# Kernel optimization log

Hardware: AMD Instinct MI355X
Metric: run time of the kernel (lower is better)

Reference implementation:

```python
import jax, jax.numpy as jnp
import numpy as np
import math

B, S, D, H = 1, 4096, 1024, 16
HD = D // H  # head_dim = 64


def setup_inputs() -> dict:
    key = jax.random.key(0)
    ks = jax.random.split(key, 6)
    x = jax.random.normal(ks[0], (B, S, D), dtype=jnp.float32)
    # Llama-style rotary frequencies: theta = 10000^{-2i/head_dim}
    inv_freq = 1.0 / (10000.0 ** (jnp.arange(0, HD, 2, dtype=jnp.float32) / HD))  # (HD/2,)
    t = jnp.arange(S, dtype=jnp.float32)
    freqs = jnp.outer(t, inv_freq)  # (S, HD/2)
    cos = jnp.cos(freqs)
    sin = jnp.sin(freqs)
    # additive causal mask (S, S): 0 on/below diagonal, -inf above
    mask = jnp.where(jnp.tril(jnp.ones((S, S), dtype=bool)), 0.0, -jnp.inf).astype(jnp.float32)
    scale = 1.0 / math.sqrt(D)
    wq = jax.random.normal(ks[1], (D, D), dtype=jnp.float32) * scale
    wk = jax.random.normal(ks[2], (D, D), dtype=jnp.float32) * scale
    wv = jax.random.normal(ks[3], (D, D), dtype=jnp.float32) * scale
    wo = jax.random.normal(ks[4], (D, D), dtype=jnp.float32) * scale
    return {"x": x, "cos": cos, "sin": sin, "mask": mask,
            "wq": wq, "wk": wk, "wv": wv, "wo": wo, "start_pos": 0}


def _rope(t, cos, sin):
    # t: (b, s, h, hd); cos/sin: (s, hd/2). Interleaved-pair complex rotation.
    b, s, h, hd = t.shape
    tr = t.reshape(b, s, h, hd // 2, 2)
    te, to = tr[..., 0], tr[..., 1]
    c = cos[None, :, None, :]
    sn = sin[None, :, None, :]
    oe = te * c - to * sn
    oo = te * sn + to * c
    return jnp.stack([oe, oo], axis=-1).reshape(b, s, h, hd)


def reference(x, cos, sin, mask, wq, wk, wv, wo, start_pos):
    b, s, d = x.shape
    h, hd = H, HD
    # Linear layers: y = x @ W.T (torch nn.Linear convention, W is (out,in))
    xq = (x @ wq.T).reshape(b, s, h, hd)
    xk = (x @ wk.T).reshape(b, s, h, hd)
    xv = (x @ wv.T).reshape(b, s, h, hd)
    xq = _rope(xq, cos, sin)
    xk = _rope(xk, cos, sin)
    # (b, h, s, hd)
    xq = xq.transpose(0, 2, 1, 3)
    xk = xk.transpose(0, 2, 1, 3)
    xv = xv.transpose(0, 2, 1, 3)
    scores = jnp.einsum('bhqd,bhkd->bhqk', xq, xk) / math.sqrt(hd)
    scores = scores + mask[None, None, :, :]
    attn = jax.nn.softmax(scores.astype(jnp.float32), axis=-1).astype(xq.dtype)
    out = jnp.einsum('bhqk,bhkd->bhqd', attn, xv)
    out = out.transpose(0, 2, 1, 3).reshape(b, s, d)
    return out @ wo.T
```

## Files before the change

kernel.cpp:

```cpp
#include <hip/hip_runtime.h>
#include <hip/hip_bf16.h>
#include <math.h>

typedef __bf16 bf16;
typedef __bf16 bf16x4 __attribute__((ext_vector_type(4)));
typedef __bf16 bf16x8 __attribute__((ext_vector_type(8)));
typedef float floatx4 __attribute__((ext_vector_type(4)));
typedef short short4v __attribute__((ext_vector_type(4)));

#define S_LEN 4096
#define DM 1024
#define NH 16
#define HD 64

#define GM 4096
#define GN 1024
#define GK 1024
#define FST 68

#define GLDS16(gp, lp) __builtin_amdgcn_global_load_lds( \
    (const __attribute__((address_space(1))) void*)(gp), \
    (__attribute__((address_space(3))) void*)(lp), 16, 0, 0)

__global__ void cvt_bf16(const float* __restrict__ x,  const float* __restrict__ wq,
                         const float* __restrict__ wk, const float* __restrict__ wv,
                         const float* __restrict__ wo, bf16* __restrict__ dst)
{
    size_t i4 = ((size_t)blockIdx.x * 256 + threadIdx.x) * 4;
    const float* src; size_t off;
    const size_t M1 = (size_t)1 << 20;
    if      (i4 < 4 * M1) { src = x;  off = i4;          }
    else if (i4 < 5 * M1) { src = wq; off = i4 - 4 * M1; }
    else if (i4 < 6 * M1) { src = wk; off = i4 - 5 * M1; }
    else if (i4 < 7 * M1) { src = wv; off = i4 - 6 * M1; }
    else                  { src = wo; off = i4 - 7 * M1; }
    float4 v = *(const float4*)(src + off);
    bf16x4 o = { (bf16)v.x, (bf16)v.y, (bf16)v.z, (bf16)v.w };
    *(bf16x4*)(&dst[i4]) = o;
}

template <typename CT>
__launch_bounds__(256)
__global__ void gemm_bt3(const bf16* __restrict__ A,
                         const bf16* __restrict__ B0, const bf16* __restrict__ B1,
                         const bf16* __restrict__ B2,
                         CT* __restrict__ C0, CT* __restrict__ C1, CT* __restrict__ C2)
{
    const int bz = blockIdx.z;
    const bf16* __restrict__ B = (bz == 0) ? B0 : (bz == 1 ? B1 : B2);
    CT* __restrict__ C         = (bz == 0) ? C0 : (bz == 1 ? C1 : C2);

    const int tid  = threadIdx.x;
    const int wave = tid >> 6;
    const int lane = tid & 63;
    const int wm   = (wave >> 1) * 64;
    const int wn   = (wave & 1) * 64;
    const int lrow = lane >> 4;
    const int lcol = lane & 15;

    const int m0 = blockIdx.y * 128;
    const int n0 = blockIdx.x * 128;

    __shared__ __align__(16) bf16 As[128 * 64];
    __shared__ __align__(16) bf16 Bs[128 * 64];

    floatx4 acc[4][4];
    #pragma unroll
    for (int i = 0; i < 4; i++)
        #pragma unroll
        for (int j = 0; j < 4; j++) acc[i][j] = (floatx4){0.f, 0.f, 0.f, 0.f};

    const bf16* ga0 = A + (size_t)(m0 + wave * 32 + (lane >> 3)) * GK + (lane & 7) * 8;
    const bf16* gb0 = B + (size_t)(n0 + wave * 32 + (lane >> 3)) * GK + (lane & 7) * 8;
    bf16* la = &As[(wave * 32) * 64];
    bf16* lb = &Bs[(wave * 32) * 64];

    for (int kt = 0; kt < GK; kt += 64) {
        #pragma unroll
        for (int i = 0; i < 4; i++) {
            GLDS16(ga0 + kt + (size_t)i * 8 * GK, la + i * 8 * 64);
            GLDS16(gb0 + kt + (size_t)i * 8 * GK, lb + i * 8 * 64);
        }
        __syncthreads();
        #pragma unroll
        for (int ks = 0; ks < 2; ks++) {
            bf16x8 af[4], bfr[4];
            #pragma unroll
            for (int t = 0; t < 4; t++) {
                af[t]  = *(const bf16x8*)(&As[(wm + t * 16 + lcol) * 64 + ks * 32 + lrow * 8]);
                bfr[t] = *(const bf16x8*)(&Bs[(wn + t * 16 + lcol) * 64 + ks * 32 + lrow * 8]);
            }
            #pragma unroll
            for (int mt = 0; mt < 4; mt++)
                #pragma unroll
                for (int nt = 0; nt < 4; nt++)
                    acc[mt][nt] = __builtin_amdgcn_mfma_f32_16x16x32_bf16(af[mt], bfr[nt], acc[mt][nt], 0, 0, 0);
        }
        __syncthreads();
    }

    #pragma unroll
    for (int mt = 0; mt < 4; mt++)
        #pragma unroll
        for (int nt = 0; nt < 4; nt++)
            #pragma unroll
            for (int r = 0; r < 4; r++) {
                int row = m0 + wm + mt * 16 + lrow * 4 + r;
                int col = n0 + wn + nt * 16 + lcol;
                C[(size_t)row * GN + col] = (CT)(acc[mt][nt][r]);
            }
}

__global__ void rope_kernel(bf16* __restrict__ Q, bf16* __restrict__ Kp,
                            const float* __restrict__ cosp, const float* __restrict__ sinp)
{
    int idx = blockIdx.x * 256 + threadIdx.x;
    int s = idx >> 9;
    int r = idx & 511;
    int h = r >> 5;
    int i = r & 31;
    float c  = cosp[s * 32 + i];
    float sn = sinp[s * 32 + i];
    int base = s * DM + h * 64 + 2 * i;
    float qe = (float)Q[base], qo = (float)Q[base + 1];
    Q[base]      = (bf16)(qe * c - qo * sn);
    Q[base + 1]  = (bf16)(qe * sn + qo * c);
    float ke = (float)Kp[base], ko = (float)Kp[base + 1];
    Kp[base]     = (bf16)(ke * c - ko * sn);
    Kp[base + 1] = (bf16)(ke * sn + ko * c);
}

__global__ void vtrans_kernel(const bf16* __restrict__ V, bf16* __restrict__ VT)
{
    __shared__ bf16 T[64 * 70];
    const int tid = threadIdx.x;
    const int s0  = blockIdx.x * 64;
    const int h   = blockIdx.y;
    #pragma unroll
    for (int i = 0; i < 2; i++) {
        int idx = i * 256 + tid;
        int r   = idx >> 3;
        int c   = (idx & 7) * 8;
        *(uint4*)(&T[r * 70 + c]) = *(const uint4*)(&V[(size_t)(s0 + r) * DM + h * 64 + c]);
    }
    __syncthreads();
    #pragma unroll
    for (int i = 0; i < 2; i++) {
        int idx = i * 256 + tid;
        int d   = idx >> 3;
        int c0  = (idx & 7) * 8;
        bf16x8 o;
        #pragma unroll
        for (int j = 0; j < 8; j++) o[j] = T[(c0 + j) * 70 + d];
        *(bf16x8*)(&VT[(size_t)(h * 64 + d) * S_LEN + s0 + c0]) = o;
    }
}

__launch_bounds__(256, 4)
__global__ void flash_attn(const bf16* __restrict__ Q, const bf16* __restrict__ K,
                           const bf16* __restrict__ VT,
                           float* __restrict__ O0, float* __restrict__ O1,
                           float* __restrict__ L0, float* __restrict__ L1)
{
    const int pi   = blockIdx.x >> 1;
    const int p    = blockIdx.x & 1;
    const int h    = blockIdx.y;
    const int tid  = threadIdx.x;
    const int wave = tid >> 6;
    const int lane = tid & 63;
    const int lrow = lane >> 4;
    const int lcol = lane & 15;

    const int qtA = pi;
    const int qtB = 63 - pi;

    float* __restrict__ Op = p ? O1 : O0;
    float* __restrict__ Lp = p ? L1 : L0;

    __shared__ __align__(16) bf16 Ks[2][64 * FST];
    __shared__ __align__(16) bf16 Vs[2][64 * FST];

    const float sc2 = 0.125f * 1.44269504088896340736f;

    const int q0A = qtA * 64 + wave * 16;
    const int q0B = qtB * 64 + wave * 16;

    const bf16* qpA = Q + (size_t)(q0A + lcol) * DM + h * HD;
    const bf16* qpB = Q + (size_t)(q0B + lcol) * DM + h * HD;
    bf16x8 qfA[2], qfB[2];
    qfA[0] = *(const bf16x8*)(qpA + 0 + lrow * 8);
    qfA[1] = *(const bf16x8*)(qpA + 32 + lrow * 8);
    qfB[0] = *(const bf16x8*)(qpB + 0 + lrow * 8);
    qfB[1] = *(const bf16x8*)(qpB + 32 + lrow * 8);

    float lA = 0.f, lB = 0.f;
    floatx4 oaccA[4], oaccB[4];
    #pragma unroll
    for (int nt = 0; nt < 4; nt++) {
        oaccA[nt] = (floatx4){0.f, 0.f, 0.f, 0.f};
        oaccB[nt] = (floatx4){0.f, 0.f, 0.f, 0.f};
    }

    const int  srow = tid >> 3;
    const int  sch  = (tid & 7) * 8;
    const bf16* kp  = K  + (size_t)srow * DM + h * HD + sch;
    const bf16* vp  = VT + (size_t)(h * HD + srow) * S_LEN + sch;
    const int  wof  = srow * FST + sch;

    {
        size_t ko = (size_t)p * 64 * DM;
        size_t vo = (size_t)p * 64;
        uint4 a = *(const uint4*)(kp + ko);
        uint4 b = *(const uint4*)(kp + ko + (size_t)32 * DM);
        uint4 c = *(const uint4*)(vp + vo);
        uint4 d = *(const uint4*)(vp + vo + (size_t)32 * S_LEN);
        *(uint4*)(&Ks[0][wof])            = a;
        *(uint4*)(&Ks[0][wof + 32 * FST]) = b;
        *(uint4*)(&Vs[0][wof])            = c;
        *(uint4*)(&Vs[0][wof + 32 * FST]) = d;
    }
    __syncthreads();

    uint4 kr0, kr1, vr0, vr1;
    for (int t = p; t <= qtB; t += 2) {
        const int  cur  = ((t - p) >> 1) & 1;
        const bool more = (t + 2 <= qtB);
        const bool actA = (t <= qtA);

        if (more) {
            size_t ko = (size_t)(t + 2) * 64 * DM;
            size_t vo = (size_t)(t + 2) * 64;
            kr0 = *(const uint4*)(kp + ko);
            kr1 = *(const uint4*)(kp + ko + (size_t)32 * DM);
            vr0 = *(const uint4*)(vp + vo);
            vr1 = *(const uint4*)(vp + vo + (size_t)32 * S_LEN);
        }

        short4v pbA[4], pbB[4];
        const bool diagA = (t == qtA);
        const bool diagB = (t == qtB);
        #pragma unroll
        for (int nt = 0; nt < 4; nt++) {
            floatx4 zB = (floatx4){0.f, 0.f, 0.f, 0.f};
            floatx4 zA = (floatx4){0.f, 0.f, 0.f, 0.f};
            #pragma unroll
            for (int ks = 0; ks < 2; ks++) {
                bf16x8 kf = *(const bf16x8*)(&Ks[cur][(nt * 16 + lcol) * FST + ks * 32 + lrow * 8]);
                zB = __builtin_amdgcn_mfma_f32_16x16x32_bf16(kf, qfB[ks], zB, 0, 0, 0);
                if (actA)
                    zA = __builtin_amdgcn_mfma_f32_16x16x32_bf16(kf, qfA[ks], zA, 0, 0, 0);
            }
            if (diagB) {
                #pragma unroll
                for (int r = 0; r < 4; r++) {
                    int kg = t * 64 + nt * 16 + lrow * 4 + r;
                    float pr = exp2f(zB[r] * sc2);
                    if (kg > q0B + lcol) pr = 0.f;
                    zB[r] = pr; lB += pr;
                }
            } else {
                #pragma unroll
                for (int r = 0; r < 4; r++) {
                    float pr = exp2f(zB[r] * sc2);
                    zB[r] = pr; lB += pr;
                }
            }
            bf16x4 pvB = { (bf16)zB[0], (bf16)zB[1], (bf16)zB[2], (bf16)zB[3] };
            pbB[nt] = __builtin_bit_cast(short4v, pvB);
            if (actA) {
                if (diagA) {
                    #pragma unroll
                    for (int r = 0; r < 4; r++) {
                        int kg = t * 64 + nt * 16 + lrow * 4 + r;
                        float pr = exp2f(zA[r] * sc2);
                        if (kg > q0A + lcol) pr = 0.f;
                        zA[r] = pr; lA += pr;
                    }
                } else {
                    #pragma unroll
                    for (int r = 0; r < 4; r++) {
                        float pr = exp2f(zA[r] * sc2);
                        zA[r] = pr; lA += pr;
                    }
                }
                bf16x4 pvA = { (bf16)zA[0], (bf16)zA[1], (bf16)zA[2], (bf16)zA[3] };
                pbA[nt] = __builtin_bit_cast(short4v, pvA);
            }
        }

        #pragma unroll
        for (int nt = 0; nt < 4; nt++)
            #pragma unroll
            for (int kt = 0; kt < 4; kt++) {
                bf16x4 va = *(const bf16x4*)(&Vs[cur][(nt * 16 + lcol) * FST + kt * 16 + lrow * 4]);
                short4v vas = __builtin_bit_cast(short4v, va);
                oaccB[nt] = __builtin_amdgcn_mfma_f32_16x16x16bf16_1k(vas, pbB[kt], oaccB[nt], 0, 0, 0);
                if (actA)
                    oaccA[nt] = __builtin_amdgcn_mfma_f32_16x16x16bf16_1k(vas, pbA[kt], oaccA[nt], 0, 0, 0);
            }

        if (more) {
            int nxt = cur ^ 1;
            *(uint4*)(&Ks[nxt][wof])            = kr0;
            *(uint4*)(&Ks[nxt][wof + 32 * FST]) = kr1;
            *(uint4*)(&Vs[nxt][wof])            = vr0;
            *(uint4*)(&Vs[nxt][wof + 32 * FST]) = vr1;
        }
        __syncthreads();
    }

    lA += __shfl_xor(lA, 16, 64);
    lA += __shfl_xor(lA, 32, 64);
    lB += __shfl_xor(lB, 16, 64);
    lB += __shfl_xor(lB, 32, 64);
    if (lrow == 0) {
        Lp[h * S_LEN + q0A + lcol] = lA;
        Lp[h * S_LEN + q0B + lcol] = lB;
    }
    #pragma unroll
    for (int nt = 0; nt < 4; nt++) {
        *(floatx4*)(&Op[(size_t)(q0A + lcol) * DM + h * HD + nt * 16 + lrow * 4]) = oaccA[nt];
        *(floatx4*)(&Op[(size_t)(q0B + lcol) * DM + h * HD + nt * 16 + lrow * 4]) = oaccB[nt];
    }
}

__global__ void combine_kernel(const float* __restrict__ O0, const float* __restrict__ O1,
                               const float* __restrict__ L0, const float* __restrict__ L1,
                               bf16* __restrict__ Aw)
{
    int i4 = (blockIdx.x * 256 + threadIdx.x) * 4;
    int q = i4 >> 10;
    int c = i4 & 1023;
    int h = c >> 6;
    float rl = 1.f / (L0[h * S_LEN + q] + L1[h * S_LEN + q]);
    float4 a = *(const float4*)(O0 + i4);
    float4 b = *(const float4*)(O1 + i4);
    bf16x4 o = { (bf16)((a.x + b.x) * rl), (bf16)((a.y + b.y) * rl),
                 (bf16)((a.z + b.z) * rl), (bf16)((a.w + b.w) * rl) };
    *(bf16x4*)(&Aw[i4]) = o;
}

extern "C" void kernel_launch(void* const* d_in, const int* in_sizes, int n_in,
                              void* d_out, int out_size, void* d_ws, size_t ws_size,
                              hipStream_t stream) {
    const float* x    = (const float*)d_in[0];
    const float* cosp = (const float*)d_in[1];
    const float* sinp = (const float*)d_in[2];
    const float* wq   = (const float*)d_in[4];
    const float* wk   = (const float*)d_in[5];
    const float* wv   = (const float*)d_in[6];
    const float* wo   = (const float*)d_in[7];
    float* out = (float*)d_out;

    const size_t SD = (size_t)S_LEN * DM;
    const size_t DD = (size_t)DM * DM;
    bf16* xb  = (bf16*)d_ws;
    bf16* wqb = xb + SD;
    bf16* wkb = wqb + DD;
    bf16* wvb = wkb + DD;
    bf16* wob = wvb + DD;
    bf16* Qw  = wob + DD;
    bf16* Kw  = Qw + SD;
    bf16* Vw  = Kw + SD;
    bf16* Aw  = Vw + SD;
    bf16* VTw = Aw + SD;
    float* O0f = (float*)(VTw + SD);
    float* O1f = O0f + SD;
    float* L0f = O1f + SD;
    float* L1f = L0f + (size_t)S_LEN * NH;

    cvt_bf16<<<8192, 256, 0, stream>>>(x, wq, wk, wv, wo, xb);
    gemm_bt3<bf16><<<dim3(GN / 128, GM / 128, 3), 256, 0, stream>>>(
        xb, wqb, wkb, wvb, Qw, Kw, Vw);
    rope_kernel<<<(S_LEN * NH * 32) / 256, 256, 0, stream>>>(Qw, Kw, cosp, sinp);
    vtrans_kernel<<<dim3(S_LEN / 64, NH), 256, 0, stream>>>(Vw, VTw);
    flash_attn<<<dim3(64, NH), 256, 0, stream>>>(Qw, Kw, VTw, O0f, O1f, L0f, L1f);
    combine_kernel<<<S_LEN * DM / 1024, 256, 0, stream>>>(O0f, O1f, L0f, L1f, Aw);
    gemm_bt3<float><<<dim3(GN / 128, GM / 128, 1), 256, 0, stream>>>(
        Aw, wob, wob, wob, out, out, out);
}
```

Baseline: 306.9 us.

## Fuse bf16 conversion, RoPE, V transpose and split combine into GEMM kernels

Removes the separate fp32-to-bf16 conversion, RoPE, V-transpose and split-combine kernels. The QKV GEMM now loads fp32 inputs and converts them while staging to padded LDS, applies RoPE in its epilogue using lane shuffles, and writes V already transposed. The output GEMM merges the two flash partials and normalises by L during its A-tile load. This saves launches and intermediate memory traffic, but gives up the async global_load_lds path and reads twice the bytes (fp32) per tile, and each weight tile is reconverted by many blocks.

```diff
diff --git a/kernel.cpp b/kernel.cpp
--- a/kernel.cpp
+++ b/kernel.cpp
@@ -16,39 +16,24 @@
 #define GM 4096
 #define GN 1024
 #define GK 1024
+#define LDST 72
 #define FST 68
 
-#define GLDS16(gp, lp) __builtin_amdgcn_global_load_lds( \
-    (const __attribute__((address_space(1))) void*)(gp), \
-    (__attribute__((address_space(3))) void*)(lp), 16, 0, 0)
-
-__global__ void cvt_bf16(const float* __restrict__ x,  const float* __restrict__ wq,
-                         const float* __restrict__ wk, const float* __restrict__ wv,
-                         const float* __restrict__ wo, bf16* __restrict__ dst)
-{
-    size_t i4 = ((size_t)blockIdx.x * 256 + threadIdx.x) * 4;
-    const float* src; size_t off;
-    const size_t M1 = (size_t)1 << 20;
-    if      (i4 < 4 * M1) { src = x;  off = i4;          }
-    else if (i4 < 5 * M1) { src = wq; off = i4 - 4 * M1; }
-    else if (i4 < 6 * M1) { src = wk; off = i4 - 5 * M1; }
-    else if (i4 < 7 * M1) { src = wv; off = i4 - 6 * M1; }
-    else                  { src = wo; off = i4 - 7 * M1; }
-    float4 v = *(const float4*)(src + off);
-    bf16x4 o = { (bf16)v.x, (bf16)v.y, (bf16)v.z, (bf16)v.w };
-    *(bf16x4*)(&dst[i4]) = o;
-}
-
-template <typename CT>
+__device__ __forceinline__ bf16x8 cvt8(float4 a, float4 b) {
+    return (bf16x8){ (bf16)a.x, (bf16)a.y, (bf16)a.z, (bf16)a.w,
+                     (bf16)b.x, (bf16)b.y, (bf16)b.z, (bf16)b.w };
+}
+
 __launch_bounds__(256)
-__global__ void gemm_bt3(const bf16* __restrict__ A,
-                         const bf16* __restrict__ B0, const bf16* __restrict__ B1,
-                         const bf16* __restrict__ B2,
-                         CT* __restrict__ C0, CT* __restrict__ C1, CT* __restrict__ C2)
+__global__ void gemm_qkv(const float* __restrict__ x,
+                         const float* __restrict__ wq, const float* __restrict__ wk,
+                         const float* __restrict__ wv,
+                         const float* __restrict__ cosp, const float* __restrict__ sinp,
+                         bf16* __restrict__ Qw, bf16* __restrict__ Kw,
+                         bf16* __restrict__ VTw)
 {
     const int bz = blockIdx.z;
-    const bf16* __restrict__ B = (bz == 0) ? B0 : (bz == 1 ? B1 : B2);
-    CT* __restrict__ C         = (bz == 0) ? C0 : (bz == 1 ? C1 : C2);
+    const float* __restrict__ B = (bz == 0) ? wq : (bz == 1 ? wk : wv);
 
     const int tid  = threadIdx.x;
     const int wave = tid >> 6;
@@ -61,8 +46,8 @@
     const int m0 = blockIdx.y * 128;
     const int n0 = blockIdx.x * 128;
 
-    __shared__ __align__(16) bf16 As[128 * 64];
-    __shared__ __align__(16) bf16 Bs[128 * 64];
+    __shared__ __align__(16) bf16 As[128 * LDST];
+    __shared__ __align__(16) bf16 Bs[128 * LDST];
 
     floatx4 acc[4][4];
     #pragma unroll
@@ -70,16 +55,18 @@
         #pragma unroll
         for (int j = 0; j < 4; j++) acc[i][j] = (floatx4){0.f, 0.f, 0.f, 0.f};
 
-    const bf16* ga0 = A + (size_t)(m0 + wave * 32 + (lane >> 3)) * GK + (lane & 7) * 8;
-    const bf16* gb0 = B + (size_t)(n0 + wave * 32 + (lane >> 3)) * GK + (lane & 7) * 8;
-    bf16* la = &As[(wave * 32) * 64];
-    bf16* lb = &Bs[(wave * 32) * 64];
-
     for (int kt = 0; kt < GK; kt += 64) {
         #pragma unroll
         for (int i = 0; i < 4; i++) {
-            GLDS16(ga0 + kt + (size_t)i * 8 * GK, la + i * 8 * 64);
-            GLDS16(gb0 + kt + (size_t)i * 8 * GK, lb + i * 8 * 64);
+            int idx = i * 256 + tid;
+            int row = idx >> 3;
+            int ch  = (idx & 7) * 8;
+            const float* ap = &x[(size_t)(m0 + row) * GK + kt + ch];
+            const float* bp = &B[(size_t)(n0 + row) * GK + kt + ch];
+            float4 a0 = *(const float4*)(ap), a1 = *(const float4*)(ap + 4);
+            float4 b0 = *(const float4*)(bp), b1 = *(const float4*)(bp + 4);
+            *(bf16x8*)(&As[row * LDST + ch]) = cvt8(a0, a1);
+            *(bf16x8*)(&Bs[row * LDST + ch]) = cvt8(b0, b1);
         }
         __syncthreads();
         #pragma unroll
@@ -87,8 +74,8 @@
             bf16x8 af[4], bfr[4];
             #pragma unroll
             for (int t = 0; t < 4; t++) {
-                af[t]  = *(const bf16x8*)(&As[(wm + t * 16 + lcol) * 64 + ks * 32 + lrow * 8]);
-                bfr[t] = *(const bf16x8*)(&Bs[(wn + t * 16 + lcol) * 64 + ks * 32 + lrow * 8]);
+                af[t]  = *(const bf16x8*)(&As[(wm + t * 16 + lcol) * LDST + ks * 32 + lrow * 8]);
+                bfr[t] = *(const bf16x8*)(&Bs[(wn + t * 16 + lcol) * LDST + ks * 32 + lrow * 8]);
             }
             #pragma unroll
             for (int mt = 0; mt < 4; mt++)
@@ -99,60 +86,36 @@
         __syncthreads();
     }
 
-    #pragma unroll
-    for (int mt = 0; mt < 4; mt++)
-        #pragma unroll
-        for (int nt = 0; nt < 4; nt++)
-            #pragma unroll
-            for (int r = 0; r < 4; r++) {
-                int row = m0 + wm + mt * 16 + lrow * 4 + r;
+    if (bz < 2) {
+        bf16* __restrict__ C = bz ? Kw : Qw;
+        const bool odd = (lcol & 1);
+        #pragma unroll
+        for (int mt = 0; mt < 4; mt++)
+            #pragma unroll
+            for (int nt = 0; nt < 4; nt++) {
+                int i = (nt * 16 + lcol) >> 1;
+                #pragma unroll
+                for (int r = 0; r < 4; r++) {
+                    float v  = acc[mt][nt][r];
+                    float pv = __shfl_xor(v, 1, 64);
+                    int s = m0 + wm + mt * 16 + lrow * 4 + r;
+                    float c  = cosp[s * 32 + i];
+                    float sn = sinp[s * 32 + i];
+                    float ov = odd ? (pv * sn + v * c) : (v * c - pv * sn);
+                    C[(size_t)s * GN + n0 + wn + nt * 16 + lcol] = (bf16)ov;
+                }
+            }
+    } else {
+        #pragma unroll
+        for (int mt = 0; mt < 4; mt++)
+            #pragma unroll
+            for (int nt = 0; nt < 4; nt++) {
                 int col = n0 + wn + nt * 16 + lcol;
-                C[(size_t)row * GN + col] = (CT)(acc[mt][nt][r]);
-            }
-}
-
-__global__ void rope_kernel(bf16* __restrict__ Q, bf16* __restrict__ Kp,
-                            const float* __restrict__ cosp, const float* __restrict__ sinp)
-{
-    int idx = blockIdx.x * 256 + threadIdx.x;
-    int s = idx >> 9;
-    int r = idx & 511;
-    int h = r >> 5;
-    int i = r & 31;
-    float c  = cosp[s * 32 + i];
-    float sn = sinp[s * 32 + i];
-    int base = s * DM + h * 64 + 2 * i;
-    float qe = (float)Q[base], qo = (float)Q[base + 1];
-    Q[base]      = (bf16)(qe * c - qo * sn);
-    Q[base + 1]  = (bf16)(qe * sn + qo * c);
-    float ke = (float)Kp[base], ko = (float)Kp[base + 1];
-    Kp[base]     = (bf16)(ke * c - ko * sn);
-    Kp[base + 1] = (bf16)(ke * sn + ko * c);
-}
-
-__global__ void vtrans_kernel(const bf16* __restrict__ V, bf16* __restrict__ VT)
-{
-    __shared__ bf16 T[64 * 70];
-    const int tid = threadIdx.x;
-    const int s0  = blockIdx.x * 64;
-    const int h   = blockIdx.y;
-    #pragma unroll
-    for (int i = 0; i < 2; i++) {
-        int idx = i * 256 + tid;
-        int r   = idx >> 3;
-        int c   = (idx & 7) * 8;
-        *(uint4*)(&T[r * 70 + c]) = *(const uint4*)(&V[(size_t)(s0 + r) * DM + h * 64 + c]);
-    }
-    __syncthreads();
-    #pragma unroll
-    for (int i = 0; i < 2; i++) {
-        int idx = i * 256 + tid;
-        int d   = idx >> 3;
-        int c0  = (idx & 7) * 8;
-        bf16x8 o;
-        #pragma unroll
-        for (int j = 0; j < 8; j++) o[j] = T[(c0 + j) * 70 + d];
-        *(bf16x8*)(&VT[(size_t)(h * 64 + d) * S_LEN + s0 + c0]) = o;
+                int s   = m0 + wm + mt * 16 + lrow * 4;
+                bf16x4 ov = { (bf16)acc[mt][nt][0], (bf16)acc[mt][nt][1],
+                              (bf16)acc[mt][nt][2], (bf16)acc[mt][nt][3] };
+                *(bf16x4*)(&VTw[(size_t)col * S_LEN + s]) = ov;
+            }
     }
 }
 
@@ -324,20 +287,81 @@
     }
 }
 
-__global__ void combine_kernel(const float* __restrict__ O0, const float* __restrict__ O1,
-                               const float* __restrict__ L0, const float* __restrict__ L1,
-                               bf16* __restrict__ Aw)
+__launch_bounds__(256)
+__global__ void gemm_out(const float* __restrict__ O0, const float* __restrict__ O1,
+                         const float* __restrict__ L0, const float* __restrict__ L1,
+                         const float* __restrict__ wo, float* __restrict__ out)
 {
-    int i4 = (blockIdx.x * 256 + threadIdx.x) * 4;
-    int q = i4 >> 10;
-    int c = i4 & 1023;
-    int h = c >> 6;
-    float rl = 1.f / (L0[h * S_LEN + q] + L1[h * S_LEN + q]);
-    float4 a = *(const float4*)(O0 + i4);
-    float4 b = *(const float4*)(O1 + i4);
-    bf16x4 o = { (bf16)((a.x + b.x) * rl), (bf16)((a.y + b.y) * rl),
-                 (bf16)((a.z + b.z) * rl), (bf16)((a.w + b.w) * rl) };
-    *(bf16x4*)(&Aw[i4]) = o;
+    const int tid  = threadIdx.x;
+    const int wave = tid >> 6;
+    const int lane = tid & 63;
+    const int wm   = (wave >> 1) * 64;
+    const int wn   = (wave & 1) * 64;
+    const int lrow = lane >> 4;
+    const int lcol = lane & 15;
+
+    const int m0 = blockIdx.y * 128;
+    const int n0 = blockIdx.x * 128;
+
+    __shared__ __align__(16) bf16 As[128 * LDST];
+    __shared__ __align__(16) bf16 Bs[128 * LDST];
+
+    floatx4 acc[4][4];
+    #pragma unroll
+    for (int i = 0; i < 4; i++)
+        #pragma unroll
+        for (int j = 0; j < 4; j++) acc[i][j] = (floatx4){0.f, 0.f, 0.f, 0.f};
+
+    for (int kt = 0; kt < GK; kt += 64) {
+        #pragma unroll
+        for (int i = 0; i < 4; i++) {
+            int idx = i * 256 + tid;
+            int row = idx >> 3;
+            int ch  = (idx & 7) * 8;
+            int s   = m0 + row;
+            int hh  = (kt + ch) >> 6;
+            float rl = 1.f / (L0[hh * S_LEN + s] + L1[hh * S_LEN + s]);
+            const float* a0p = &O0[(size_t)s * GK + kt + ch];
+            const float* a1p = &O1[(size_t)s * GK + kt + ch];
+            float4 a0 = *(const float4*)(a0p), a1 = *(const float4*)(a0p + 4);
+            float4 b0 = *(const float4*)(a1p), b1 = *(const float4*)(a1p + 4);
+            bf16x8 av = { (bf16)((a0.x + b0.x) * rl), (bf16)((a0.y + b0.y) * rl),
+                          (bf16)((a0.z + b0.z) * rl), (bf16)((a0.w + b0.w) * rl),
+                          (bf16)((a1.x + b1.x) * rl), (bf16)((a1.y + b1.y) * rl),
+                          (bf16)((a1.z + b1.z) * rl), (bf16)((a1.w + b1.w) * rl) };
+            *(bf16x8*)(&As[row * LDST + ch]) = av;
+            const float* bp = &wo[(size_t)(n0 + row) * GK + kt + ch];
+            float4 w0 = *(const float4*)(bp), w1 = *(const float4*)(bp + 4);
+            *(bf16x8*)(&Bs[row * LDST + ch]) = cvt8(w0, w1);
+        }
+        __syncthreads();
+        #pragma unroll
+        for (int ks = 0; ks < 2; ks++) {
+            bf16x8 af[4], bfr[4];
+            #pragma unroll
+            for (int t = 0; t < 4; t++) {
+                af[t]  = *(const bf16x8*)(&As[(wm + t * 16 + lcol) * LDST + ks * 32 + lrow * 8]);
+                bfr[t] = *(const bf16x8*)(&Bs[(wn + t * 16 + lcol) * LDST + ks * 32 + lrow * 8]);
+            }
+            #pragma unroll
+            for (int mt = 0; mt < 4; mt++)
+                #pragma unroll
+                for (int nt = 0; nt < 4; nt++)
+                    acc[mt][nt] = __builtin_amdgcn_mfma_f32_16x16x32_bf16(af[mt], bfr[nt], acc[mt][nt], 0, 0, 0);
+        }
+        __syncthreads();
+    }
+
+    #pragma unroll
+    for (int mt = 0; mt < 4; mt++)
+        #pragma unroll
+        for (int nt = 0; nt < 4; nt++)
+            #pragma unroll
+            for (int r = 0; r < 4; r++) {
+                int row = m0 + wm + mt * 16 + lrow * 4 + r;
+                int col = n0 + wn + nt * 16 + lcol;
+                out[(size_t)row * GN + col] = acc[mt][nt][r];
+            }
 }
 
 extern "C" void kernel_launch(void* const* d_in, const int* in_sizes, int n_in,
@@ -353,29 +377,17 @@
     float* out = (float*)d_out;
 
     const size_t SD = (size_t)S_LEN * DM;
-    const size_t DD = (size_t)DM * DM;
-    bf16* xb  = (bf16*)d_ws;
-    bf16* wqb = xb + SD;
-    bf16* wkb = wqb + DD;
-    bf16* wvb = wkb + DD;
-    bf16* wob = wvb + DD;
-    bf16* Qw  = wob + DD;
+    bf16* Qw  = (bf16*)d_ws;
     bf16* Kw  = Qw + SD;
-    bf16* Vw  = Kw + SD;
-    bf16* Aw  = Vw + SD;
-    bf16* VTw = Aw + SD;
+    bf16* VTw = Kw + SD;
     float* O0f = (float*)(VTw + SD);
     float* O1f = O0f + SD;
     float* L0f = O1f + SD;
     float* L1f = L0f + (size_t)S_LEN * NH;
 
-    cvt_bf16<<<8192, 256, 0, stream>>>(x, wq, wk, wv, wo, xb);
-    gemm_bt3<bf16><<<dim3(GN / 128, GM / 128, 3), 256, 0, stream>>>(
-        xb, wqb, wkb, wvb, Qw, Kw, Vw);
-    rope_kernel<<<(S_LEN * NH * 32) / 256, 256, 0, stream>>>(Qw, Kw, cosp, sinp);
-    vtrans_kernel<<<dim3(S_LEN / 64, NH), 256, 0, stream>>>(Vw, VTw);
+    gemm_qkv<<<dim3(GN / 128, GM / 128, 3), 256, 0, stream>>>(
+        x, wq, wk, wv, cosp, sinp, Qw, Kw, VTw);
     flash_attn<<<dim3(64, NH), 256, 0, stream>>>(Qw, Kw, VTw, O0f, O1f, L0f, L1f);
-    combine_kernel<<<S_LEN * DM / 1024, 256, 0, stream>>>(O0f, O1f, L0f, L1f, Aw);
-    gemm_bt3<float><<<dim3(GN / 128, GM / 128, 1), 256, 0, stream>>>(
-        Aw, wob, wob, wob, out, out, out);
-}
+    gemm_out<<<dim3(GN / 128, GM / 128, 1), 256, 0, stream>>>(
+        O0f, O1f, L0f, L1f, wo, out);
+}
```

Result: slower. 336.4 us (+9.6%).
